# Optimization experiments

Measured on AMD Instinct MI355X. Metric: run time of the kernel, lower is better.

Reference implementation:

```python
import jax, jax.numpy as jnp
import numpy as np


def ste_sign(w):
    # larq ste_sign: forward sign(w) with sign(0)=+1; backward = identity clipped to |w|<=1.
    s = jnp.where(w >= 0, 1.0, -1.0).astype(w.dtype)
    c = jnp.clip(w, -1.0, 1.0)
    return c + jax.lax.stop_gradient(s - c)


def setup_inputs() -> dict:
    key = jax.random.key(0)
    k1, k2, k3 = jax.random.split(key, 3)
    B, H, W, Cin, Cout, NCLS = 512, 64, 64, 1, 32, 10
    x = jax.random.normal(k1, (B, H, W, Cin), dtype=jnp.float32)
    conv_w = jax.random.normal(k2, (3, 3, Cin, Cout), dtype=jnp.float32) * 0.5
    conv_b = jnp.zeros((Cout,), dtype=jnp.float32)
    dense_w = jax.random.normal(k3, (Cout, NCLS), dtype=jnp.float32) * 0.1
    dense_b = jnp.zeros((NCLS,), dtype=jnp.float32)
    return {"x": x, "conv_w": conv_w, "conv_b": conv_b,
            "dense_w": dense_w, "dense_b": dense_b}


def reference(x, conv_w, conv_b, dense_w, dense_b):
    # Binarized conv (weights quantized to +-1), SAME padding, stride 1.
    wq = ste_sign(conv_w)  # [3,3,1,32]
    y = jax.lax.conv_general_dilated(
        x, wq, window_strides=(1, 1), padding="SAME",
        dimension_numbers=("NHWC", "HWIO", "NHWC"))
    y = y + conv_b  # [B,64,64,32]
    # Global average pool over H,W -> [B,32]
    p = jnp.mean(y, axis=(1, 2))
    # Dense + softmax -> [B,10]
    logits = p @ dense_w + dense_b
    return jax.nn.softmax(logits, axis=-1)
```

## Files before the change

### kernel.cpp

```cpp
#include <hip/hip_runtime.h>
#include <math.h>


__global__ __launch_bounds__(256) void binconv_fused(
    const float* __restrict__ x,
    const float* __restrict__ conv_w,
    const float* __restrict__ conv_b,
    const float* __restrict__ dense_w,
    const float* __restrict__ dense_b,
    float* __restrict__ out)
{
    const int b = blockIdx.x;
    const int tid = threadIdx.x;
    const float* img = x + (size_t)b * 4096;
    const float4* img4 = (const float4*)img;

    float tot = 0.f, top = 0.f, bot = 0.f, lef = 0.f, rig = 0.f;
#pragma unroll
    for (int it = 0; it < 4; ++it) {
        int i = it * 256 + tid;
        float4 v = img4[i];
        float s4 = (v.x + v.y) + (v.z + v.w);
        int r  = i >> 4;
        int c0 = (i & 15) << 2;
        tot += s4;
        if (r == 0)   top += s4;
        if (r == 63)  bot += s4;
        if (c0 == 0)  lef += v.x;
        if (c0 == 60) rig += v.w;
    }

#pragma unroll
    for (int off = 32; off; off >>= 1) {
        tot += __shfl_xor(tot, off);
        top += __shfl_xor(top, off);
        bot += __shfl_xor(bot, off);
        lef += __shfl_xor(lef, off);
        rig += __shfl_xor(rig, off);
    }

    __shared__ float wsum[4][5];
    __shared__ float Msh[9][10];
    __shared__ float biassh[10];

    const int wave = tid >> 6, lane = tid & 63;
    if (lane == 0) {
        wsum[wave][0] = tot; wsum[wave][1] = top; wsum[wave][2] = bot;
        wsum[wave][3] = lef; wsum[wave][4] = rig;
    }

    if (tid < 90) {
        const int k = tid / 10, j = tid % 10;
        float m = 0.f;
#pragma unroll
        for (int c = 0; c < 32; ++c) {
            float w = conv_w[k * 32 + c];
            float s = (w >= 0.f) ? 1.f : -1.f;
            m += s * dense_w[c * 10 + j];
        }
        Msh[k][j] = m;
    } else if (tid < 100) {
        const int j = tid - 90;
        float bsum = dense_b[j];
        for (int c = 0; c < 32; ++c) bsum += conv_b[c] * dense_w[c * 10 + j];
        biassh[j] = bsum;
    }
    __syncthreads();

    if (tid == 0) {
        float T  = wsum[0][0] + wsum[1][0] + wsum[2][0] + wsum[3][0];
        float Rt = wsum[0][1] + wsum[1][1] + wsum[2][1] + wsum[3][1];
        float Rb = wsum[0][2] + wsum[1][2] + wsum[2][2] + wsum[3][2];
        float Cl = wsum[0][3] + wsum[1][3] + wsum[2][3] + wsum[3][3];
        float Cr = wsum[0][4] + wsum[1][4] + wsum[2][4] + wsum[3][4];
        const float x00 = img[0];
        const float x0e = img[63];
        const float xe0 = img[63 * 64];
        const float xee = img[63 * 64 + 63];

        float S[9];
#pragma unroll
        for (int dh = 0; dh < 3; ++dh) {
#pragma unroll
            for (int dw = 0; dw < 3; ++dw) {
                float s = T;
                if (dh == 0) s -= Rb;
                if (dh == 2) s -= Rt;
                if (dw == 0) s -= Cr;
                if (dw == 2) s -= Cl;
                if (dh == 0 && dw == 0) s += xee;
                if (dh == 0 && dw == 2) s += xe0;
                if (dh == 2 && dw == 0) s += x0e;
                if (dh == 2 && dw == 2) s += x00;
                S[dh * 3 + dw] = s;
            }
        }

        float logits[10];
        float mx = -1e30f;
#pragma unroll
        for (int j = 0; j < 10; ++j) {
            float acc = 0.f;
#pragma unroll
            for (int k = 0; k < 9; ++k) acc += S[k] * Msh[k][j];
            acc = acc * (1.f / 4096.f) + biassh[j];
            logits[j] = acc;
            mx = fmaxf(mx, acc);
        }
        float se = 0.f;
#pragma unroll
        for (int j = 0; j < 10; ++j) { logits[j] = expf(logits[j] - mx); se += logits[j]; }
        const float inv = 1.f / se;
        float* o = out + b * 10;
#pragma unroll
        for (int j = 0; j < 10; ++j) o[j] = logits[j] * inv;
    }
}

extern "C" void kernel_launch(void* const* d_in, const int* in_sizes, int n_in,
                              void* d_out, int out_size, void* d_ws, size_t ws_size,
                              hipStream_t stream) {
    const float* x       = (const float*)d_in[0];
    const float* conv_w  = (const float*)d_in[1];
    const float* conv_b  = (const float*)d_in[2];
    const float* dense_w = (const float*)d_in[3];
    const float* dense_b = (const float*)d_in[4];
    float* out = (float*)d_out;
    binconv_fused<<<512, 256, 0, stream>>>(x, conv_w, conv_b, dense_w, dense_b, out);
}
```

Before: 66.97 us.

## Use single-wave blocks with register-held image and wave-parallel softmax

Each 64-thread block now handles one image, issuing all 16 float4 loads per lane up front and reducing through wave shuffles alone, with no cross-wave shared-memory reduction. Corner values come from lane shuffles instead of extra global loads. The 9x10 folded weight matrix is computed by two passes over the single wave, and logits plus softmax are spread across 10 lanes using shuffle reductions, replacing the single-thread serial tail. The cost is fewer threads per block, so overall memory-level parallelism relies on more loads in flight per lane and on block-level occupancy.

```diff
diff --git a/kernel.cpp b/kernel.cpp
--- a/kernel.cpp
+++ b/kernel.cpp
@@ -2,7 +2,7 @@
 #include <math.h>
 
 
-__global__ __launch_bounds__(256) void binconv_fused(
+__global__ __launch_bounds__(64) void binconv_fused(
     const float* __restrict__ x,
     const float* __restrict__ conv_w,
     const float* __restrict__ conv_b,
@@ -11,24 +11,70 @@
     float* __restrict__ out)
 {
     const int b = blockIdx.x;
-    const int tid = threadIdx.x;
-    const float* img = x + (size_t)b * 4096;
-    const float4* img4 = (const float4*)img;
+    const int t = threadIdx.x;
+    const float4* img4 = (const float4*)(x + (size_t)b * 4096);
+
+    float4 v[16];
+#pragma unroll
+    for (int k = 0; k < 16; ++k) v[k] = img4[k * 64 + t];
+
+    __shared__ float MB[100];
+    {
+        const int t0 = t;
+        float r0 = 0.f;
+        if (t0 < 90) {
+            const int k = t0 / 10, j = t0 % 10;
+#pragma unroll 8
+            for (int c = 0; c < 32; ++c) {
+                const float dw = dense_w[c * 10 + j];
+                r0 += (conv_w[k * 32 + c] >= 0.f) ? dw : -dw;
+            }
+        } else {
+            const int j = t0 - 90;
+            r0 = dense_b[j];
+#pragma unroll 8
+            for (int c = 0; c < 32; ++c) r0 += conv_b[c] * dense_w[c * 10 + j];
+        }
+        MB[t0] = r0;
+
+        const int t1 = t + 64;
+        if (t1 < 100) {
+            float r1 = 0.f;
+            if (t1 < 90) {
+                const int k = t1 / 10, j = t1 % 10;
+#pragma unroll 8
+                for (int c = 0; c < 32; ++c) {
+                    const float dw = dense_w[c * 10 + j];
+                    r1 += (conv_w[k * 32 + c] >= 0.f) ? dw : -dw;
+                }
+            } else {
+                const int j = t1 - 90;
+                r1 = dense_b[j];
+#pragma unroll 8
+                for (int c = 0; c < 32; ++c) r1 += conv_b[c] * dense_w[c * 10 + j];
+            }
+            MB[t1] = r1;
+        }
+    }
 
     float tot = 0.f, top = 0.f, bot = 0.f, lef = 0.f, rig = 0.f;
+    const int cg = t & 15;
+    const int rg = t >> 4;
 #pragma unroll
-    for (int it = 0; it < 4; ++it) {
-        int i = it * 256 + tid;
-        float4 v = img4[i];
-        float s4 = (v.x + v.y) + (v.z + v.w);
-        int r  = i >> 4;
-        int c0 = (i & 15) << 2;
+    for (int k = 0; k < 16; ++k) {
+        const float4 vv = v[k];
+        const float s4 = (vv.x + vv.y) + (vv.z + vv.w);
         tot += s4;
-        if (r == 0)   top += s4;
-        if (r == 63)  bot += s4;
-        if (c0 == 0)  lef += v.x;
-        if (c0 == 60) rig += v.w;
+        if (k == 0 && rg == 0)  top += s4;
+        if (k == 15 && rg == 3) bot += s4;
+        if (cg == 0)  lef += vv.x;
+        if (cg == 15) rig += vv.w;
     }
+    float corn = 0.f;
+    if (t == 0)  corn = v[0].x;
+    if (t == 15) corn = v[0].w;
+    if (t == 48) corn = v[15].x;
+    if (t == 63) corn = v[15].w;
 
 #pragma unroll
     for (int off = 32; off; off >>= 1) {
@@ -38,83 +84,55 @@
         lef += __shfl_xor(lef, off);
         rig += __shfl_xor(rig, off);
     }
+    const float x00 = __shfl(corn, 0);
+    const float x0e = __shfl(corn, 15);
+    const float xe0 = __shfl(corn, 48);
+    const float xee = __shfl(corn, 63);
 
-    __shared__ float wsum[4][5];
-    __shared__ float Msh[9][10];
-    __shared__ float biassh[10];
+    __syncthreads();
 
-    const int wave = tid >> 6, lane = tid & 63;
-    if (lane == 0) {
-        wsum[wave][0] = tot; wsum[wave][1] = top; wsum[wave][2] = bot;
-        wsum[wave][3] = lef; wsum[wave][4] = rig;
+    float S[9];
+#pragma unroll
+    for (int dh = 0; dh < 3; ++dh) {
+#pragma unroll
+        for (int dw = 0; dw < 3; ++dw) {
+            float s = tot;
+            if (dh == 0) s -= bot;
+            if (dh == 2) s -= top;
+            if (dw == 0) s -= rig;
+            if (dw == 2) s -= lef;
+            if (dh == 0 && dw == 0) s += xee;
+            if (dh == 0 && dw == 2) s += xe0;
+            if (dh == 2 && dw == 0) s += x0e;
+            if (dh == 2 && dw == 2) s += x00;
+            S[dh * 3 + dw] = s;
+        }
     }
 
-    if (tid < 90) {
-        const int k = tid / 10, j = tid % 10;
-        float m = 0.f;
+    float m[9], bs;
+    if (t < 10) {
 #pragma unroll
-        for (int c = 0; c < 32; ++c) {
-            float w = conv_w[k * 32 + c];
-            float s = (w >= 0.f) ? 1.f : -1.f;
-            m += s * dense_w[c * 10 + j];
-        }
-        Msh[k][j] = m;
-    } else if (tid < 100) {
-        const int j = tid - 90;
-        float bsum = dense_b[j];
-        for (int c = 0; c < 32; ++c) bsum += conv_b[c] * dense_w[c * 10 + j];
-        biassh[j] = bsum;
+        for (int k = 0; k < 9; ++k) m[k] = MB[k * 10 + t];
+        bs = MB[90 + t];
+    } else {
+#pragma unroll
+        for (int k = 0; k < 9; ++k) m[k] = 0.f;
+        bs = -1e30f;
     }
-    __syncthreads();
+    float acc = 0.f;
+#pragma unroll
+    for (int k = 0; k < 9; ++k) acc += S[k] * m[k];
+    const float logit = acc * (1.f / 4096.f) + bs;
 
-    if (tid == 0) {
-        float T  = wsum[0][0] + wsum[1][0] + wsum[2][0] + wsum[3][0];
-        float Rt = wsum[0][1] + wsum[1][1] + wsum[2][1] + wsum[3][1];
-        float Rb = wsum[0][2] + wsum[1][2] + wsum[2][2] + wsum[3][2];
-        float Cl = wsum[0][3] + wsum[1][3] + wsum[2][3] + wsum[3][3];
-        float Cr = wsum[0][4] + wsum[1][4] + wsum[2][4] + wsum[3][4];
-        const float x00 = img[0];
-        const float x0e = img[63];
-        const float xe0 = img[63 * 64];
-        const float xee = img[63 * 64 + 63];
-
-        float S[9];
+    float mx = logit;
 #pragma unroll
-        for (int dh = 0; dh < 3; ++dh) {
+    for (int off = 8; off; off >>= 1) mx = fmaxf(mx, __shfl_xor(mx, off));
+    const float ex = expf(logit - mx);
+    float se = ex;
 #pragma unroll
-            for (int dw = 0; dw < 3; ++dw) {
-                float s = T;
-                if (dh == 0) s -= Rb;
-                if (dh == 2) s -= Rt;
-                if (dw == 0) s -= Cr;
-                if (dw == 2) s -= Cl;
-                if (dh == 0 && dw == 0) s += xee;
-                if (dh == 0 && dw == 2) s += xe0;
-                if (dh == 2 && dw == 0) s += x0e;
-                if (dh == 2 && dw == 2) s += x00;
-                S[dh * 3 + dw] = s;
-            }
-        }
-
-        float logits[10];
-        float mx = -1e30f;
-#pragma unroll
-        for (int j = 0; j < 10; ++j) {
-            float acc = 0.f;
-#pragma unroll
-            for (int k = 0; k < 9; ++k) acc += S[k] * Msh[k][j];
-            acc = acc * (1.f / 4096.f) + biassh[j];
-            logits[j] = acc;
-            mx = fmaxf(mx, acc);
-        }
-        float se = 0.f;
-#pragma unroll
-        for (int j = 0; j < 10; ++j) { logits[j] = expf(logits[j] - mx); se += logits[j]; }
-        const float inv = 1.f / se;
-        float* o = out + b * 10;
-#pragma unroll
-        for (int j = 0; j < 10; ++j) o[j] = logits[j] * inv;
-    }
+    for (int off = 8; off; off >>= 1) se += __shfl_xor(se, off);
+    const float inv = 1.f / se;
+    if (t < 10) out[b * 10 + t] = ex * inv;
 }
 
 extern "C" void kernel_launch(void* const* d_in, const int* in_sizes, int n_in,
@@ -126,5 +144,5 @@
     const float* dense_w = (const float*)d_in[3];
     const float* dense_b = (const float*)d_in[4];
     float* out = (float*)d_out;
-    binconv_fused<<<512, 256, 0, stream>>>(x, conv_w, conv_b, dense_w, dense_b, out);
+    binconv_fused<<<512, 64, 0, stream>>>(x, conv_w, conv_b, dense_w, dense_b, out);
 }
```

Measured after the change: 67.28 us. No clear change (+0.5%).
